# Kernel tuning notes

Hardware: AMD Instinct MI355X
Metric: run time of the kernel (lower is better)

Reference implementation:

```python
import jax, jax.numpy as jnp
import numpy as np

B, S, D, H = 2, 2048, 1024, 16
HD = D // H  # head_dim = 64


def _rope_cos_sin(seq_len, head_dim, base=10000.0):
    # theta_i = base^(-2*(i-1)/dim), i = 1..dim/2
    i = jnp.arange(head_dim // 2, dtype=jnp.float32)
    theta = base ** (-2.0 * i / head_dim)
    m = jnp.arange(seq_len, dtype=jnp.float32)
    ang = jnp.outer(m, theta)  # [S, HD/2]
    return jnp.cos(ang), jnp.sin(ang)


def _apply_rope(x, cos, sin):
    # x: [B, S, H, HD]; pairs are consecutive elements (view_as_complex on (..., HD/2, 2))
    xr = x[..., 0::2]
    xi = x[..., 1::2]
    c = cos[None, :, None, :]
    s = sin[None, :, None, :]
    out_r = xr * c - xi * s
    out_i = xr * s + xi * c
    return jnp.stack([out_r, out_i], axis=-1).reshape(x.shape)


def setup_inputs() -> dict:
    key = jax.random.key(0)
    ks = jax.random.split(key, 7)
    sc = 1.0 / np.sqrt(D)
    return {
        "x": jax.random.normal(ks[0], (B, S, D), dtype=jnp.float32),
        "wq_w": jax.random.normal(ks[1], (D, D), dtype=jnp.float32) * sc,
        "wq_b": jax.random.normal(ks[2], (D,), dtype=jnp.float32) * 0.01,
        "wk_w": jax.random.normal(ks[3], (D, D), dtype=jnp.float32) * sc,
        "wk_b": jax.random.normal(ks[4], (D,), dtype=jnp.float32) * 0.01,
        "wv_w": jax.random.normal(ks[5], (D, D), dtype=jnp.float32) * sc,
        "wv_b": jax.random.normal(ks[6], (D,), dtype=jnp.float32) * 0.01,
    }


def reference(x, wq_w, wq_b, wk_w, wk_b, wv_w, wv_b):
    bs, seq_len, dim = x.shape
    # torch Linear: y = x @ W^T + b
    xq = (x @ wq_w.T + wq_b).reshape(bs, seq_len, H, HD)
    xk = (x @ wk_w.T + wk_b).reshape(bs, seq_len, H, HD)
    xv = (x @ wv_w.T + wv_b).reshape(bs, seq_len, H, HD)
    # RoPE (inference=True, start_pos=0): freqs for first seq_len positions
    cos, sin = _rope_cos_sin(seq_len, HD)
    xq = _apply_rope(xq, cos, sin)
    xk = _apply_rope(xk, cos, sin)
    # naive attention with full [B,H,S,S] score matrix, as in the original
    q = xq.transpose(0, 2, 1, 3)  # [B,H,S,HD]
    k = xk.transpose(0, 2, 1, 3)
    v = xv.transpose(0, 2, 1, 3)
    scores = jnp.einsum("bhqd,bhkd->bhqk", q, k) / np.sqrt(HD)
    attn = jax.nn.softmax(scores.astype(jnp.float32), axis=-1)
    out = jnp.einsum("bhqk,bhkd->bhqd", attn, v)
    return out.transpose(0, 2, 1, 3).reshape(bs, seq_len, dim)
```

## Files before the change

kernel.cpp:

```cpp
#include <hip/hip_runtime.h>


typedef __bf16 bf16;
typedef bf16  bf16x8 __attribute__((ext_vector_type(8)));
typedef bf16  bf16x4 __attribute__((ext_vector_type(4)));
typedef float f32x4  __attribute__((ext_vector_type(4)));
typedef float f32x16 __attribute__((ext_vector_type(16)));

typedef const __attribute__((address_space(1))) void* gptr_t;
typedef __attribute__((address_space(3))) void*       sptr_t;

__device__ __forceinline__ void gload_lds16(const void* g, void* l) {
  __builtin_amdgcn_global_load_lds((gptr_t)g, (sptr_t)l, 16, 0, 0);
}

__global__ __launch_bounds__(256) void prep_kernel(
    const float* __restrict__ x, const float* __restrict__ wq,
    const float* __restrict__ wk, const float* __restrict__ wv,
    bf16* __restrict__ xb, bf16* __restrict__ wqb, bf16* __restrict__ wkb,
    bf16* __restrict__ wvb, float* __restrict__ ctab, float* __restrict__ stab) {
  int g = blockIdx.x * 256 + threadIdx.x;
  const float* src;
  bf16* dst;
  int i;
  if (g < 1048576) { src = x; dst = xb; i = g; }
  else if (g < 1310720) { src = wq; dst = wqb; i = g - 1048576; }
  else if (g < 1572864) { src = wk; dst = wkb; i = g - 1310720; }
  else if (g < 1835008) { src = wv; dst = wvb; i = g - 1572864; }
  else {
    int idx = g - 1835008;
    if (idx < 65536) {
      int s = idx >> 5, p = idx & 31;
      double theta = exp2(-(double)p * (13.287712379549449 / 32.0));
      double ang = (double)s * theta;
      ctab[idx] = (float)cos(ang);
      stab[idx] = (float)sin(ang);
    }
    return;
  }
  const float4 v = reinterpret_cast<const float4*>(src)[i];
  bf16x4 o;
  o[0] = (bf16)v.x; o[1] = (bf16)v.y; o[2] = (bf16)v.z; o[3] = (bf16)v.w;
  reinterpret_cast<bf16x4*>(dst)[i] = o;
}

__global__ __launch_bounds__(256) void qkv_gemm_kernel(
    const bf16* __restrict__ xb, const bf16* __restrict__ wqb,
    const bf16* __restrict__ wkb, const bf16* __restrict__ wvb,
    const float* __restrict__ bq, const float* __restrict__ bk2,
    const float* __restrict__ bv, const float* __restrict__ ctab,
    const float* __restrict__ stab, bf16* __restrict__ qb,
    bf16* __restrict__ kb, bf16* __restrict__ vb) {
  const int z = blockIdx.z;
  const bf16* W = (z == 0) ? wqb : (z == 1) ? wkb : wvb;
  const float* bias = (z == 0) ? bq : (z == 1) ? bk2 : bv;
  bf16* dst = (z == 0) ? qb : (z == 1) ? kb : vb;

  __shared__ bf16 As[128 * 32];
  __shared__ bf16 Bs[128 * 32];

  const int tid = threadIdx.x;
  const int wid = tid >> 6;
  const int l = tid & 63;
  const int lg = l >> 4, lc = l & 15;
  const int wr = wid >> 1, wc = wid & 1;
  const int m0 = blockIdx.x * 128, n0 = blockIdx.y * 128;

  f32x4 acc[4][4] = {};

  const int arow = tid >> 2;
  const int acol = (tid & 3) * 8;
  const bf16* asrc = xb + (size_t)(m0 + arow) * 1024 + acol;
  const bf16* bsrc = W + (size_t)(n0 + arow) * 1024 + acol;
  char* alds = (char*)As + wid * 1024;
  char* blds = (char*)Bs + wid * 1024;

  for (int k0 = 0; k0 < 1024; k0 += 32) {
    gload_lds16(asrc + k0, alds);
    gload_lds16(asrc + 64 * 1024 + k0, alds + 4096);
    gload_lds16(bsrc + k0, blds);
    gload_lds16(bsrc + 64 * 1024 + k0, blds + 4096);
    __syncthreads();
    bf16x8 af[4], bfr[4];
#pragma unroll
    for (int i = 0; i < 4; ++i)
      af[i] = *reinterpret_cast<const bf16x8*>(
          (const char*)As + ((wr * 64 + i * 16 + lc) * 64 + lg * 16));
#pragma unroll
    for (int j = 0; j < 4; ++j)
      bfr[j] = *reinterpret_cast<const bf16x8*>(
          (const char*)Bs + ((wc * 64 + j * 16 + lc) * 64 + lg * 16));
#pragma unroll
    for (int i = 0; i < 4; ++i)
#pragma unroll
      for (int j = 0; j < 4; ++j)
        acc[i][j] = __builtin_amdgcn_mfma_f32_16x16x32_bf16(af[i], bfr[j],
                                                            acc[i][j], 0, 0, 0);
    __syncthreads();
  }

#pragma unroll
  for (int i = 0; i < 4; ++i)
#pragma unroll
    for (int j = 0; j < 4; ++j) {
      const int nb = n0 + wc * 64 + j * 16 + lc;
      const float bval = bias[nb];
#pragma unroll
      for (int r = 0; r < 4; ++r) {
        const int m = m0 + wr * 64 + i * 16 + lg * 4 + r;
        const float val = acc[i][j][r] + bval;
        if (z == 2) {
          dst[(size_t)m * 1024 + nb] = (bf16)val;
        } else {
          const int s = m & 2047;
          const int pi = (nb & 63) >> 1;
          const float c = ctab[s * 32 + pi];
          const float sn = stab[s * 32 + pi];
          const float part = __shfl_xor(val, 1, 64);
          float res = (nb & 1) ? fmaf(part, sn, val * c)
                               : fmaf(-part, sn, val * c);
          if (z == 0) res *= 0.18033688011112042f;
          dst[(size_t)m * 1024 + nb] = (bf16)res;
        }
      }
    }
}

__global__ __launch_bounds__(256) void vtrans_kernel(const bf16* __restrict__ vb,
                                                     bf16* __restrict__ vt) {
  __shared__ bf16 tile[64][65];
  const int bh = blockIdx.y, b = bh >> 4, h = bh & 15;
  const int s0 = blockIdx.x * 64;
  const int t = threadIdx.x;
#pragma unroll
  for (int idx = t; idx < 4096; idx += 256) {
    int r = idx >> 6, c = idx & 63;
    tile[r][c] = vb[(size_t)(b * 2048 + s0 + r) * 1024 + h * 64 + c];
  }
  __syncthreads();
#pragma unroll
  for (int idx = t; idx < 4096; idx += 256) {
    int d = idx >> 6, r = idx & 63;
    vt[(size_t)(bh * 64 + d) * 2048 + s0 + r] = tile[r][d];
  }
}

__device__ __forceinline__ unsigned pkbf(float a, float b) {
  union { bf16 h[2]; unsigned u; } t;
  t.h[0] = (bf16)a; t.h[1] = (bf16)b;
  return t.u;
}

__global__ __launch_bounds__(256) void attn_kernel(const bf16* __restrict__ qb,
                                                   const bf16* __restrict__ kb,
                                                   const bf16* __restrict__ vt,
                                                   float* __restrict__ out) {
  __shared__ bf16 Kt[2][64][64];
  __shared__ bf16 Vt[2][64][64];

  const int tid = threadIdx.x;
  const int wid = tid >> 6;
  const int l = tid & 63;
  const int lc = l & 31;
  const int hi = l >> 5;
  const int bid = blockIdx.x;
  const int swz = (bid & 7) * 64 + (bid >> 3);
  const int bh = swz >> 4;
  const int qt = swz & 15;
  const int b = bh >> 4, h = bh & 15;
  const int q0 = qt * 128 + wid * 32;

  const bf16* Q = qb + (size_t)(b * 2048 + q0) * 1024 + h * 64;
  const bf16* K = kb + (size_t)(b * 2048) * 1024 + h * 64;
  const bf16* V = vt + (size_t)bh * 64 * 2048;

  bf16x8 qf[4];
#pragma unroll
  for (int md = 0; md < 4; ++md)
    qf[md] = *reinterpret_cast<const bf16x8*>(Q + (size_t)lc * 1024 + md * 16 + hi * 8);

  const int srow = l >> 3;
  const int schk = (l & 7) ^ (srow & 7);
  const bf16* ksrc0 = K + (size_t)(wid * 16 + srow) * 1024 + schk * 8;
  const bf16* ksrc1 = ksrc0 + (size_t)8 * 1024;
  const bf16* vsrc0 = V + (size_t)(wid * 16 + srow) * 2048 + schk * 8;
  const bf16* vsrc1 = vsrc0 + (size_t)8 * 2048;

  f32x16 o0 = {};
  f32x16 o1 = {};
  float mrun = -1e30f, lrun = 0.f;
  const int sb = (hi ^ 1) * 2;
  const int swzk = lc & 7;

  gload_lds16(ksrc0, &Kt[0][wid * 16][0]);
  gload_lds16(ksrc1, &Kt[0][wid * 16 + 8][0]);
  gload_lds16(vsrc0, &Vt[0][wid * 16][0]);
  gload_lds16(vsrc1, &Vt[0][wid * 16 + 8][0]);
  __syncthreads();

  int bb = 0;
  for (int kt0 = 0; kt0 < 32; ++kt0) {
    if (kt0 < 31) {
      const size_t ko = (size_t)(kt0 + 1) * 64 * 1024;
      const size_t vo = (size_t)(kt0 + 1) * 64;
      gload_lds16(ksrc0 + ko, &Kt[bb ^ 1][wid * 16][0]);
      gload_lds16(ksrc1 + ko, &Kt[bb ^ 1][wid * 16 + 8][0]);
      gload_lds16(vsrc0 + vo, &Vt[bb ^ 1][wid * 16][0]);
      gload_lds16(vsrc1 + vo, &Vt[bb ^ 1][wid * 16 + 8][0]);
    }
#pragma unroll
    for (int sub = 0; sub < 2; ++sub) {
      f32x16 s = {};
#pragma unroll
      for (int md = 0; md < 4; ++md) {
        bf16x8 kf = *reinterpret_cast<const bf16x8*>(
            &Kt[bb][sub * 32 + lc][(((md << 1) | hi) ^ swzk) << 3]);
        s = __builtin_amdgcn_mfma_f32_32x32x16_bf16(kf, qf[md], s, 0, 0, 0);
      }

      float tm = s[0];
#pragma unroll
      for (int r = 1; r < 16; ++r) tm = fmaxf(tm, s[r]);
      tm = fmaxf(tm, __shfl_xor(tm, 32, 64));
      if (!__all(tm <= mrun + 8.0f)) {
        const float mn = fmaxf(mrun, tm);
        const float corr = exp2f(mrun - mn);
        mrun = mn;
        lrun *= corr;
#pragma unroll
        for (int r = 0; r < 16; ++r) { o0[r] *= corr; o1[r] *= corr; }
      }
      float ts = 0.f;
#pragma unroll
      for (int r = 0; r < 16; ++r) {
        s[r] = exp2f(s[r] - mrun);
        ts += s[r];
      }
      ts += __shfl_xor(ts, 32, 64);
      lrun += ts;

      unsigned pw[8];
#pragma unroll
      for (int w = 0; w < 8; ++w) pw[w] = pkbf(s[2 * w], s[2 * w + 1]);

      unsigned rx0 = __shfl_xor(pw[sb + 0], 32, 64);
      unsigned rx1 = __shfl_xor(pw[sb + 1], 32, 64);
      unsigned rx2 = __shfl_xor(pw[4 + sb + 0], 32, 64);
      unsigned rx3 = __shfl_xor(pw[4 + sb + 1], 32, 64);

      union { unsigned u[4]; bf16x8 v; } bf0, bf1;
      if (hi == 0) {
        bf0.u[0] = pw[0]; bf0.u[1] = pw[1]; bf0.u[2] = rx0; bf0.u[3] = rx1;
        bf1.u[0] = pw[4]; bf1.u[1] = pw[5]; bf1.u[2] = rx2; bf1.u[3] = rx3;
      } else {
        bf0.u[0] = rx0; bf0.u[1] = rx1; bf0.u[2] = pw[2]; bf0.u[3] = pw[3];
        bf1.u[0] = rx2; bf1.u[1] = rx3; bf1.u[2] = pw[6]; bf1.u[3] = pw[7];
      }

      const int vc = sub * 4 + hi;
      bf16x8 vf00 = *reinterpret_cast<const bf16x8*>(
          &Vt[bb][lc][((vc ^ swzk)) << 3]);
      bf16x8 vf01 = *reinterpret_cast<const bf16x8*>(
          &Vt[bb][lc][(((vc + 2) ^ swzk)) << 3]);
      bf16x8 vf10 = *reinterpret_cast<const bf16x8*>(
          &Vt[bb][lc + 32][((vc ^ swzk)) << 3]);
      bf16x8 vf11 = *reinterpret_cast<const bf16x8*>(
          &Vt[bb][lc + 32][(((vc + 2) ^ swzk)) << 3]);
      o0 = __builtin_amdgcn_mfma_f32_32x32x16_bf16(vf00, bf0.v, o0, 0, 0, 0);
      o0 = __builtin_amdgcn_mfma_f32_32x32x16_bf16(vf01, bf1.v, o0, 0, 0, 0);
      o1 = __builtin_amdgcn_mfma_f32_32x32x16_bf16(vf10, bf0.v, o1, 0, 0, 0);
      o1 = __builtin_amdgcn_mfma_f32_32x32x16_bf16(vf11, bf1.v, o1, 0, 0, 0);
    }
    __syncthreads();
    bb ^= 1;
  }

  const float inv = 1.f / lrun;
  float* orow = out + (size_t)(b * 2048 + q0 + lc) * 1024 + h * 64;
#pragma unroll
  for (int g = 0; g < 4; ++g) {
    f32x4 v0, v1;
#pragma unroll
    for (int e = 0; e < 4; ++e) { v0[e] = o0[g * 4 + e] * inv; v1[e] = o1[g * 4 + e] * inv; }
    *reinterpret_cast<f32x4*>(orow + g * 8 + 4 * hi) = v0;
    *reinterpret_cast<f32x4*>(orow + 32 + g * 8 + 4 * hi) = v1;
  }
}

extern "C" void kernel_launch(void* const* d_in, const int* in_sizes, int n_in,
                              void* d_out, int out_size, void* d_ws, size_t ws_size,
                              hipStream_t stream) {
  const float* x  = (const float*)d_in[0];
  const float* wq = (const float*)d_in[1];
  const float* bq = (const float*)d_in[2];
  const float* wk = (const float*)d_in[3];
  const float* bk = (const float*)d_in[4];
  const float* wv = (const float*)d_in[5];
  const float* bv = (const float*)d_in[6];
  float* out = (float*)d_out;

  char* ws = (char*)d_ws;
  bf16* xb  = (bf16*)(ws);
  bf16* wqb = (bf16*)(ws + 8388608);
  bf16* wkb = (bf16*)(ws + 10485760);
  bf16* wvb = (bf16*)(ws + 12582912);
  bf16* qb  = (bf16*)(ws + 14680064);
  bf16* kb  = (bf16*)(ws + 23068672);
  bf16* vb  = (bf16*)(ws + 31457280);
  bf16* vt  = (bf16*)(ws + 39845888);
  float* ctab = (float*)(ws + 48234496);
  float* stab = (float*)(ws + 48496640);

  prep_kernel<<<7424, 256, 0, stream>>>(x, wq, wk, wv, xb, wqb, wkb, wvb,
                                        ctab, stab);

  qkv_gemm_kernel<<<dim3(32, 8, 3), 256, 0, stream>>>(
      xb, wqb, wkb, wvb, bq, bk, bv, ctab, stab, qb, kb, vb);

  vtrans_kernel<<<dim3(32, 32), 256, 0, stream>>>(vb, vt);

  attn_kernel<<<512, 256, 0, stream>>>(qb, kb, vt, out);
}
```

Baseline: 218.9 us.

## Fuse V transpose into QKV GEMM, widen GEMM K-tile, shrink attention blocks

The QKV GEMM now writes V directly in transposed per-head layout, which removes the separate transpose kernel and its extra round trip through global memory. The GEMM K-tile doubles to 64 and uses an XOR-swizzled LDS layout to avoid bank conflicts. The attention kernel switches to 128-thread blocks covering 64 queries, which doubles the grid, and each wave loads more of the K/V tile. It also adds s_setprio around the MFMA sections and uses inline asm for v_exp_f32, v_max3_f32 and packed bf16 conversion. The transposed V stores from the GEMM epilogue are strided and uncoalesced, and smaller attention blocks mean each K/V tile is reused by fewer queries.

```diff
diff --git a/kernel.cpp b/kernel.cpp
--- a/kernel.cpp
+++ b/kernel.cpp
@@ -12,6 +12,19 @@
 
 __device__ __forceinline__ void gload_lds16(const void* g, void* l) {
   __builtin_amdgcn_global_load_lds((gptr_t)g, (sptr_t)l, 16, 0, 0);
+}
+
+__device__ __forceinline__ float fexp2(float x) {
+  float r; asm("v_exp_f32 %0, %1" : "=v"(r) : "v"(x)); return r;
+}
+__device__ __forceinline__ float max3f(float a, float b, float c) {
+  float r; asm("v_max3_f32 %0, %1, %2, %3" : "=v"(r) : "v"(a), "v"(b), "v"(c));
+  return r;
+}
+__device__ __forceinline__ unsigned pkbf(float a, float b) {
+  unsigned r;
+  asm("v_cvt_pk_bf16_f32 %0, %1, %2" : "=v"(r) : "v"(a), "v"(b));
+  return r;
 }
 
 __global__ __launch_bounds__(256) void prep_kernel(
@@ -50,14 +63,13 @@
     const float* __restrict__ bq, const float* __restrict__ bk2,
     const float* __restrict__ bv, const float* __restrict__ ctab,
     const float* __restrict__ stab, bf16* __restrict__ qb,
-    bf16* __restrict__ kb, bf16* __restrict__ vb) {
+    bf16* __restrict__ kb, bf16* __restrict__ vt) {
   const int z = blockIdx.z;
   const bf16* W = (z == 0) ? wqb : (z == 1) ? wkb : wvb;
   const float* bias = (z == 0) ? bq : (z == 1) ? bk2 : bv;
-  bf16* dst = (z == 0) ? qb : (z == 1) ? kb : vb;
-
-  __shared__ bf16 As[128 * 32];
-  __shared__ bf16 Bs[128 * 32];
+
+  __shared__ bf16 As[128 * 64];
+  __shared__ bf16 Bs[128 * 64];
 
   const int tid = threadIdx.x;
   const int wid = tid >> 6;
@@ -68,34 +80,52 @@
 
   f32x4 acc[4][4] = {};
 
-  const int arow = tid >> 2;
-  const int acol = (tid & 3) * 8;
-  const bf16* asrc = xb + (size_t)(m0 + arow) * 1024 + acol;
-  const bf16* bsrc = W + (size_t)(n0 + arow) * 1024 + acol;
+  const int srow = tid >> 3;
+  const int schunk = (tid & 7) ^ (srow & 7);
+  const bf16* asrc = xb + (size_t)(m0 + srow) * 1024 + schunk * 8;
+  const bf16* bsrc = W + (size_t)(n0 + srow) * 1024 + schunk * 8;
   char* alds = (char*)As + wid * 1024;
   char* blds = (char*)Bs + wid * 1024;
 
-  for (int k0 = 0; k0 < 1024; k0 += 32) {
-    gload_lds16(asrc + k0, alds);
-    gload_lds16(asrc + 64 * 1024 + k0, alds + 4096);
-    gload_lds16(bsrc + k0, blds);
-    gload_lds16(bsrc + 64 * 1024 + k0, blds + 4096);
+  for (int k0 = 0; k0 < 1024; k0 += 64) {
+#pragma unroll
+    for (int i = 0; i < 4; ++i) {
+      gload_lds16(asrc + (size_t)32 * i * 1024 + k0, alds + i * 4096);
+      gload_lds16(bsrc + (size_t)32 * i * 1024 + k0, blds + i * 4096);
+    }
     __syncthreads();
-    bf16x8 af[4], bfr[4];
+    bf16x8 af[4][2], bfr[4][2];
+#pragma unroll
+    for (int i = 0; i < 4; ++i) {
+      const int row = wr * 64 + i * 16 + lc;
+#pragma unroll
+      for (int h = 0; h < 2; ++h) {
+        const int slot = (h * 4 + lg) ^ (row & 7);
+        af[i][h] = *reinterpret_cast<const bf16x8*>(
+            (const char*)As + row * 128 + slot * 16);
+      }
+    }
+#pragma unroll
+    for (int j = 0; j < 4; ++j) {
+      const int row = wc * 64 + j * 16 + lc;
+#pragma unroll
+      for (int h = 0; h < 2; ++h) {
+        const int slot = (h * 4 + lg) ^ (row & 7);
+        bfr[j][h] = *reinterpret_cast<const bf16x8*>(
+            (const char*)Bs + row * 128 + slot * 16);
+      }
+    }
+    __builtin_amdgcn_s_setprio(1);
 #pragma unroll
     for (int i = 0; i < 4; ++i)
-      af[i] = *reinterpret_cast<const bf16x8*>(
-          (const char*)As + ((wr * 64 + i * 16 + lc) * 64 + lg * 16));
-#pragma unroll
-    for (int j = 0; j < 4; ++j)
-      bfr[j] = *reinterpret_cast<const bf16x8*>(
-          (const char*)Bs + ((wc * 64 + j * 16 + lc) * 64 + lg * 16));
-#pragma unroll
-    for (int i = 0; i < 4; ++i)
-#pragma unroll
-      for (int j = 0; j < 4; ++j)
-        acc[i][j] = __builtin_amdgcn_mfma_f32_16x16x32_bf16(af[i], bfr[j],
+#pragma unroll
+      for (int j = 0; j < 4; ++j) {
+        acc[i][j] = __builtin_amdgcn_mfma_f32_16x16x32_bf16(af[i][0], bfr[j][0],
                                                             acc[i][j], 0, 0, 0);
+        acc[i][j] = __builtin_amdgcn_mfma_f32_16x16x32_bf16(af[i][1], bfr[j][1],
+                                                            acc[i][j], 0, 0, 0);
+      }
+    __builtin_amdgcn_s_setprio(0);
     __syncthreads();
   }
 
@@ -110,7 +140,8 @@
         const int m = m0 + wr * 64 + i * 16 + lg * 4 + r;
         const float val = acc[i][j][r] + bval;
         if (z == 2) {
-          dst[(size_t)m * 1024 + nb] = (bf16)val;
+          vt[((size_t)((m >> 11) * 16 + (nb >> 6)) * 64 + (nb & 63)) * 2048 +
+             (m & 2047)] = (bf16)val;
         } else {
           const int s = m & 2047;
           const int pi = (nb & 63) >> 1;
@@ -120,38 +151,14 @@
           float res = (nb & 1) ? fmaf(part, sn, val * c)
                                : fmaf(-part, sn, val * c);
           if (z == 0) res *= 0.18033688011112042f;
+          bf16* dst = (z == 0) ? qb : kb;
           dst[(size_t)m * 1024 + nb] = (bf16)res;
         }
       }
     }
 }
 
-__global__ __launch_bounds__(256) void vtrans_kernel(const bf16* __restrict__ vb,
-                                                     bf16* __restrict__ vt) {
-  __shared__ bf16 tile[64][65];
-  const int bh = blockIdx.y, b = bh >> 4, h = bh & 15;
-  const int s0 = blockIdx.x * 64;
-  const int t = threadIdx.x;
-#pragma unroll
-  for (int idx = t; idx < 4096; idx += 256) {
-    int r = idx >> 6, c = idx & 63;
-    tile[r][c] = vb[(size_t)(b * 2048 + s0 + r) * 1024 + h * 64 + c];
-  }
-  __syncthreads();
-#pragma unroll
-  for (int idx = t; idx < 4096; idx += 256) {
-    int d = idx >> 6, r = idx & 63;
-    vt[(size_t)(bh * 64 + d) * 2048 + s0 + r] = tile[r][d];
-  }
-}
-
-__device__ __forceinline__ unsigned pkbf(float a, float b) {
-  union { bf16 h[2]; unsigned u; } t;
-  t.h[0] = (bf16)a; t.h[1] = (bf16)b;
-  return t.u;
-}
-
-__global__ __launch_bounds__(256) void attn_kernel(const bf16* __restrict__ qb,
+__global__ __launch_bounds__(128) void attn_kernel(const bf16* __restrict__ qb,
                                                    const bf16* __restrict__ kb,
                                                    const bf16* __restrict__ vt,
                                                    float* __restrict__ out) {
@@ -164,11 +171,11 @@
   const int lc = l & 31;
   const int hi = l >> 5;
   const int bid = blockIdx.x;
-  const int swz = (bid & 7) * 64 + (bid >> 3);
-  const int bh = swz >> 4;
-  const int qt = swz & 15;
+  const int swz = (bid & 7) * 128 + (bid >> 3);
+  const int bh = swz >> 5;
+  const int qt = swz & 31;
   const int b = bh >> 4, h = bh & 15;
-  const int q0 = qt * 128 + wid * 32;
+  const int q0 = qt * 64 + wid * 32;
 
   const bf16* Q = qb + (size_t)(b * 2048 + q0) * 1024 + h * 64;
   const bf16* K = kb + (size_t)(b * 2048) * 1024 + h * 64;
@@ -181,10 +188,8 @@
 
   const int srow = l >> 3;
   const int schk = (l & 7) ^ (srow & 7);
-  const bf16* ksrc0 = K + (size_t)(wid * 16 + srow) * 1024 + schk * 8;
-  const bf16* ksrc1 = ksrc0 + (size_t)8 * 1024;
-  const bf16* vsrc0 = V + (size_t)(wid * 16 + srow) * 2048 + schk * 8;
-  const bf16* vsrc1 = vsrc0 + (size_t)8 * 2048;
+  const bf16* ksrc = K + (size_t)(wid * 32 + srow) * 1024 + schk * 8;
+  const bf16* vsrc = V + (size_t)(wid * 32 + srow) * 2048 + schk * 8;
 
   f32x16 o0 = {};
   f32x16 o1 = {};
@@ -192,10 +197,11 @@
   const int sb = (hi ^ 1) * 2;
   const int swzk = lc & 7;
 
-  gload_lds16(ksrc0, &Kt[0][wid * 16][0]);
-  gload_lds16(ksrc1, &Kt[0][wid * 16 + 8][0]);
-  gload_lds16(vsrc0, &Vt[0][wid * 16][0]);
-  gload_lds16(vsrc1, &Vt[0][wid * 16 + 8][0]);
+#pragma unroll
+  for (int j = 0; j < 4; ++j) {
+    gload_lds16(ksrc + (size_t)8 * j * 1024, &Kt[0][wid * 32 + 8 * j][0]);
+    gload_lds16(vsrc + (size_t)8 * j * 2048, &Vt[0][wid * 32 + 8 * j][0]);
+  }
   __syncthreads();
 
   int bb = 0;
@@ -203,28 +209,36 @@
     if (kt0 < 31) {
       const size_t ko = (size_t)(kt0 + 1) * 64 * 1024;
       const size_t vo = (size_t)(kt0 + 1) * 64;
-      gload_lds16(ksrc0 + ko, &Kt[bb ^ 1][wid * 16][0]);
-      gload_lds16(ksrc1 + ko, &Kt[bb ^ 1][wid * 16 + 8][0]);
-      gload_lds16(vsrc0 + vo, &Vt[bb ^ 1][wid * 16][0]);
-      gload_lds16(vsrc1 + vo, &Vt[bb ^ 1][wid * 16 + 8][0]);
+#pragma unroll
+      for (int j = 0; j < 4; ++j) {
+        gload_lds16(ksrc + ko + (size_t)8 * j * 1024,
+                    &Kt[bb ^ 1][wid * 32 + 8 * j][0]);
+        gload_lds16(vsrc + vo + (size_t)8 * j * 2048,
+                    &Vt[bb ^ 1][wid * 32 + 8 * j][0]);
+      }
     }
 #pragma unroll
     for (int sub = 0; sub < 2; ++sub) {
       f32x16 s = {};
+      __builtin_amdgcn_s_setprio(1);
 #pragma unroll
       for (int md = 0; md < 4; ++md) {
         bf16x8 kf = *reinterpret_cast<const bf16x8*>(
             &Kt[bb][sub * 32 + lc][(((md << 1) | hi) ^ swzk) << 3]);
         s = __builtin_amdgcn_mfma_f32_32x32x16_bf16(kf, qf[md], s, 0, 0, 0);
       }
-
-      float tm = s[0];
-#pragma unroll
-      for (int r = 1; r < 16; ++r) tm = fmaxf(tm, s[r]);
+      __builtin_amdgcn_s_setprio(0);
+
+      float t0 = max3f(s[0], s[1], s[2]);
+      float t1 = max3f(s[3], s[4], s[5]);
+      float t2 = max3f(s[6], s[7], s[8]);
+      float t3 = max3f(s[9], s[10], s[11]);
+      float t4 = max3f(s[12], s[13], s[14]);
+      float tm = fmaxf(max3f(t0, t1, t2), max3f(t3, t4, s[15]));
       tm = fmaxf(tm, __shfl_xor(tm, 32, 64));
       if (!__all(tm <= mrun + 8.0f)) {
         const float mn = fmaxf(mrun, tm);
-        const float corr = exp2f(mrun - mn);
+        const float corr = fexp2(mrun - mn);
         mrun = mn;
         lrun *= corr;
 #pragma unroll
@@ -233,7 +247,7 @@
       float ts = 0.f;
 #pragma unroll
       for (int r = 0; r < 16; ++r) {
-        s[r] = exp2f(s[r] - mrun);
+        s[r] = fexp2(s[r] - mrun);
         ts += s[r];
       }
       ts += __shfl_xor(ts, 32, 64);
@@ -266,10 +280,12 @@
           &Vt[bb][lc + 32][((vc ^ swzk)) << 3]);
       bf16x8 vf11 = *reinterpret_cast<const bf16x8*>(
           &Vt[bb][lc + 32][(((vc + 2) ^ swzk)) << 3]);
+      __builtin_amdgcn_s_setprio(1);
       o0 = __builtin_amdgcn_mfma_f32_32x32x16_bf16(vf00, bf0.v, o0, 0, 0, 0);
       o0 = __builtin_amdgcn_mfma_f32_32x32x16_bf16(vf01, bf1.v, o0, 0, 0, 0);
       o1 = __builtin_amdgcn_mfma_f32_32x32x16_bf16(vf10, bf0.v, o1, 0, 0, 0);
       o1 = __builtin_amdgcn_mfma_f32_32x32x16_bf16(vf11, bf1.v, o1, 0, 0, 0);
+      __builtin_amdgcn_s_setprio(0);
     }
     __syncthreads();
     bb ^= 1;
@@ -306,18 +322,15 @@
   bf16* wvb = (bf16*)(ws + 12582912);
   bf16* qb  = (bf16*)(ws + 14680064);
   bf16* kb  = (bf16*)(ws + 23068672);
-  bf16* vb  = (bf16*)(ws + 31457280);
-  bf16* vt  = (bf16*)(ws + 39845888);
-  float* ctab = (float*)(ws + 48234496);
-  float* stab = (float*)(ws + 48496640);
+  bf16* vt  = (bf16*)(ws + 31457280);
+  float* ctab = (float*)(ws + 39845888);
+  float* stab = (float*)(ws + 40108032);
 
   prep_kernel<<<7424, 256, 0, stream>>>(x, wq, wk, wv, xb, wqb, wkb, wvb,
                                         ctab, stab);
 
   qkv_gemm_kernel<<<dim3(32, 8, 3), 256, 0, stream>>>(
-      xb, wqb, wkb, wvb, bq, bk, bv, ctab, stab, qb, kb, vb);
-
-  vtrans_kernel<<<dim3(32, 32), 256, 0, stream>>>(vb, vt);
-
-  attn_kernel<<<512, 256, 0, stream>>>(qb, kb, vt, out);
-}
+      xb, wqb, wkb, wvb, bq, bk, bv, ctab, stab, qb, kb, vt);
+
+  attn_kernel<<<1024, 128, 0, stream>>>(qb, kb, vt, out);
+}
```

After: 227.0 us. +3.7%, slower.
